# Performance work log

Measured on AMD Instinct MI355X. Metric: run time of the kernel, lower is better.

The kernel has to match this reference:

```python
import jax, jax.numpy as jnp
import numpy as np
import math

SEQ = 16384      # total ragged tokens
DIM = 1280       # vision hidden size
HEADS = 16
HDIM = DIM // HEADS  # 80
NSEG = 16        # number of segments (images); equal lengths of 1024


def rotate_half(x):
    x1, x2 = jnp.split(x, 2, axis=-1)
    return jnp.concatenate([-x2, x1], axis=-1)


def setup_inputs() -> dict:
    key = jax.random.key(0)
    ks = jax.random.split(key, 6)
    hidden_states = jax.random.normal(ks[0], (SEQ, DIM), dtype=jnp.float32)
    # rotary tables over the full head_dim (Qwen vision style: freqs duplicated)
    inv_freq = 1.0 / (10000.0 ** (jnp.arange(0, HDIM, 2, dtype=jnp.float32) / HDIM))
    pos = jnp.arange(SEQ, dtype=jnp.float32)
    freqs = jnp.outer(pos, inv_freq)                      # [S, HDIM/2]
    emb = jnp.concatenate([freqs, freqs], axis=-1)        # [S, HDIM]
    cos, sin = jnp.cos(emb), jnp.sin(emb)
    w_qkv = jax.random.normal(ks[1], (3 * DIM, DIM), dtype=jnp.float32) * 0.02
    b_qkv = jax.random.normal(ks[2], (3 * DIM,), dtype=jnp.float32) * 0.02
    w_proj = jax.random.normal(ks[3], (DIM, DIM), dtype=jnp.float32) * 0.02
    b_proj = jax.random.normal(ks[4], (DIM,), dtype=jnp.float32) * 0.02
    cu_seqlens = jnp.arange(NSEG + 1, dtype=jnp.int32) * (SEQ // NSEG)
    return {"hidden_states": hidden_states, "cos": cos, "sin": sin,
            "w_qkv": w_qkv, "b_qkv": b_qkv, "w_proj": w_proj, "b_proj": b_proj,
            "cu_seqlens": cu_seqlens}


def reference(hidden_states, cos, sin, w_qkv, b_qkv, w_proj, b_proj, cu_seqlens):
    S, D = hidden_states.shape
    hd = cos.shape[-1]
    nh = D // hd
    nseg = cu_seqlens.shape[0] - 1
    L = S // nseg  # equal segment lengths (matches cu_seqlens built in setup)

    qkv = hidden_states @ w_qkv.T + b_qkv                 # [S, 3D]
    qkv = qkv.reshape(S, 3, nh, hd)
    q, k, v = qkv[:, 0], qkv[:, 1], qkv[:, 2]             # [S, H, hd]

    # rotary (computed in float32, as in the original)
    c = cos[:, None, :]
    s = sin[:, None, :]
    q = q * c + rotate_half(q) * s
    k = k * c + rotate_half(k) * s

    # block-diagonal attention: reshape ragged-equal segments into a batch dim
    qs = q.reshape(nseg, L, nh, hd)
    ks = k.reshape(nseg, L, nh, hd)
    vs = v.reshape(nseg, L, nh, hd)

    scale = 1.0 / math.sqrt(hd)
    scores = jnp.einsum('bqhd,bkhd->bhqk', qs, ks) * scale   # [nseg, H, L, L]
    probs = jax.nn.softmax(scores, axis=-1)
    out = jnp.einsum('bhqk,bkhd->bqhd', probs, vs)           # [nseg, L, H, hd]
    out = out.reshape(S, D)
    return out @ w_proj.T + b_proj
```

## Files before the change

### kernel.cpp

```cpp
#include <hip/hip_runtime.h>

#define SEQ 16384
#define DIM 1280
#define NH 16
#define HD 80
#define NSEG 16
#define SEGL 1024

typedef __attribute__((ext_vector_type(8))) short bf16x8;
typedef __attribute__((ext_vector_type(4))) float f32x4;

__device__ inline unsigned short f2bf(float f){
  unsigned int x = __builtin_bit_cast(unsigned int, f);
  unsigned int r = (x + 0x7FFFu + ((x >> 16) & 1u)) >> 16;
  return (unsigned short)r;
}
__device__ inline float bf2f(unsigned short u){
  unsigned int x = ((unsigned int)u) << 16;
  return __builtin_bit_cast(float, x);
}
__device__ inline int cvtpk_bf16(float lo, float hi){
  int r;
  asm("v_cvt_pk_bf16_f32 %0, %1, %2" : "=v"(r) : "v"(lo), "v"(hi));
  return r;
}

__device__ inline void gload16(const unsigned short* g, unsigned short* l){
  __builtin_amdgcn_global_load_lds((const __attribute__((address_space(1))) void*)g,
                                   (__attribute__((address_space(3))) void*)l, 16, 0, 0);
}

__global__ __launch_bounds__(256) void pack_bf16_kernel(const float* __restrict__ src,
                                                        unsigned short* __restrict__ dst, int n4){
  int i = blockIdx.x * 256 + threadIdx.x;
  if (i >= n4) return;
  float4 v = ((const float4*)src)[i];
  ushort4 o;
  o.x = f2bf(v.x); o.y = f2bf(v.y); o.z = f2bf(v.z); o.w = f2bf(v.w);
  ((ushort4*)dst)[i] = o;
}

template<int EPI>
__global__ __launch_bounds__(512, 2) void gemm256_kernel(const unsigned short* __restrict__ A,
    const unsigned short* __restrict__ B, const float* __restrict__ bias,
    void* __restrict__ Cout, int M, int N, int K){
  __shared__ __attribute__((aligned(16))) unsigned short As[2][16384];
  __shared__ __attribute__((aligned(16))) unsigned short Bs[2][16384];
  const int nwg = gridDim.x;
  int bid = blockIdx.x;
  int swz = (bid & 7) * (nwg >> 3) + (bid >> 3);
  const int ntn = N >> 8;
  const int tm = (swz / ntn) << 8;
  const int tn = (swz % ntn) << 8;
  const int tid = threadIdx.x;
  const int wid = tid >> 6, l = tid & 63;
  const int lr = l & 15, lh = l >> 4;
  const int wrM = (wid >> 2) << 7;
  const int wcN = (wid & 3) << 6;
  const int NITER = K >> 7;

  const int srow = wid*8 + (l >> 3);
  const int scol = ((l & 7) ^ (l >> 3)) << 3;
  const int sldsu = wid << 9;

  const unsigned short* Ag = A + (size_t)tm * K;
  const unsigned short* Bg = B + (size_t)tn * K;

  const int ck0 = (lh*8) ^ ((l & 7) << 3);
  const int ck1 = (32 + lh*8) ^ ((l & 7) << 3);
  const int raA = (wrM + lr) << 6;
  const int raB = (wcN + lr) << 6;

  f32x4 zf = {0.f,0.f,0.f,0.f};
  f32x4 acc[8][4];
  #pragma unroll
  for (int i=0;i<8;i++)
    #pragma unroll
    for (int j=0;j<4;j++) acc[i][j] = zf;

#define STAGE_A(tile, h, q) gload16(Ag + (size_t)((h)*128 + (q)*64 + srow)*K + ((tile)<<6) + scol, \
                                    &As[(tile)&1][(h)*8192 + (q)*4096 + sldsu])
#define STAGE_B(tile, h, q) gload16(Bg + (size_t)((h)*128 + (q)*64 + srow)*K + ((tile)<<6) + scol, \
                                    &Bs[(tile)&1][(h)*8192 + (q)*4096 + sldsu])
#define RD_A(b, MOFF) \
  _Pragma("unroll") \
  for (int mi=0; mi<4; ++mi){ \
    a[0][mi] = *(const bf16x8*)&As[b][raA + ((MOFF)+mi)*1024 + ck0]; \
    a[1][mi] = *(const bf16x8*)&As[b][raA + ((MOFF)+mi)*1024 + ck1]; }
#define RD_B(b, NOFF, BREG) \
  _Pragma("unroll") \
  for (int nj=0; nj<2; ++nj){ \
    BREG[0][nj] = *(const bf16x8*)&Bs[b][raB + ((NOFF)+nj)*1024 + ck0]; \
    BREG[1][nj] = *(const bf16x8*)&Bs[b][raB + ((NOFF)+nj)*1024 + ck1]; }
#define PH_BAR() __builtin_amdgcn_s_barrier(); \
  asm volatile("s_waitcnt lgkmcnt(0)" ::: "memory"); \
  __builtin_amdgcn_sched_barrier(0);
#define QMFMA(MB, NB, BREG) \
  __builtin_amdgcn_s_setprio(1); \
  _Pragma("unroll") \
  for (int mi=0; mi<4; ++mi){ \
    _Pragma("unroll") \
    for (int nj=0; nj<2; ++nj){ \
      acc[(MB)+mi][(NB)+nj] = __builtin_amdgcn_mfma_f32_16x16x32_bf16(a[0][mi], BREG[0][nj], acc[(MB)+mi][(NB)+nj], 0,0,0); \
      acc[(MB)+mi][(NB)+nj] = __builtin_amdgcn_mfma_f32_16x16x32_bf16(a[1][mi], BREG[1][nj], acc[(MB)+mi][(NB)+nj], 0,0,0); \
    } \
  } \
  __builtin_amdgcn_s_setprio(0); \
  __builtin_amdgcn_s_barrier();

  #pragma unroll
  for (int q=0;q<2;q++){ STAGE_A(0,0,q); }
  #pragma unroll
  for (int q=0;q<2;q++){ STAGE_A(0,1,q); }
  #pragma unroll
  for (int q=0;q<2;q++){ STAGE_B(0,0,q); }
  #pragma unroll
  for (int q=0;q<2;q++){ STAGE_B(0,1,q); }
  #pragma unroll
  for (int q=0;q<2;q++){ STAGE_B(1,0,q); }
  #pragma unroll
  for (int q=0;q<2;q++){ STAGE_B(1,1,q); }
  asm volatile("s_waitcnt vmcnt(4)" ::: "memory");
  __builtin_amdgcn_s_barrier();

  for (int i=0; i<NITER; ++i){
    const int T = 2*i;
    const bool st = (i+1 < NITER);
    bf16x8 a[2][4], bx[2][2], by[2][2];

    RD_A(0, 0); RD_B(0, 0, bx);
    STAGE_A(T+1, 0, 0); STAGE_A(T+1, 0, 1);
    PH_BAR(); QMFMA(0, 0, bx);

    RD_B(0, 2, by);
    STAGE_A(T+1, 1, 0); STAGE_A(T+1, 1, 1);
    PH_BAR(); QMFMA(0, 2, by);

    RD_A(0, 4);
    if (st){ STAGE_B(T+2, 0, 0); STAGE_B(T+2, 0, 1); }
    PH_BAR(); QMFMA(4, 2, by);

    if (st){
      STAGE_B(T+2, 1, 0); STAGE_B(T+2, 1, 1);
      asm volatile("s_waitcnt vmcnt(4)" ::: "memory");
    } else {
      asm volatile("s_waitcnt vmcnt(0)" ::: "memory");
    }
    PH_BAR(); QMFMA(4, 0, bx);

    RD_A(1, 0); RD_B(1, 0, bx);
    if (st){ STAGE_A(T+2, 0, 0); STAGE_A(T+2, 0, 1); }
    PH_BAR(); QMFMA(0, 0, bx);

    RD_B(1, 2, by);
    if (st){ STAGE_A(T+2, 1, 0); STAGE_A(T+2, 1, 1); }
    PH_BAR(); QMFMA(0, 2, by);

    RD_A(1, 4);
    if (st){ STAGE_B(T+3, 0, 0); STAGE_B(T+3, 0, 1); }
    PH_BAR(); QMFMA(4, 2, by);

    if (st){
      STAGE_B(T+3, 1, 0); STAGE_B(T+3, 1, 1);
      asm volatile("s_waitcnt vmcnt(4)" ::: "memory");
    }
    PH_BAR(); QMFMA(4, 0, bx);
  }

#undef STAGE_A
#undef STAGE_B
#undef RD_A
#undef RD_B
#undef PH_BAR
#undef QMFMA

  #pragma unroll
  for (int nj=0;nj<4;nj++){
    int col = tn + wcN + nj*16 + lr;
    float bv = bias[col];
    if (EPI == 0){
      unsigned short* Q = (unsigned short*)Cout;
      int which = col / DIM;
      int rem = col - which*DIM;
      int hh = rem / HD;
      int d = rem - hh*HD;
      size_t base = (size_t)(which*NH + hh) * SEQ;
      #pragma unroll
      for (int mi=0;mi<8;mi++){
        #pragma unroll
        for (int r=0;r<4;r++){
          int row = tm + wrM + mi*16 + lh*4 + r;
          Q[(base + row)*HD + d] = f2bf(acc[mi][nj][r] + bv);
        }
      }
    } else {
      float* C = (float*)Cout;
      #pragma unroll
      for (int mi=0;mi<8;mi++){
        #pragma unroll
        for (int r=0;r<4;r++){
          int row = tm + wrM + mi*16 + lh*4 + r;
          C[(size_t)row*N + col] = acc[mi][nj][r] + bv;
        }
      }
    }
  }
}

__global__ __launch_bounds__(256) void rope_kernel(unsigned short* __restrict__ QKV,
    const float* __restrict__ cosb, const float* __restrict__ sinb){
  unsigned int gid = blockIdx.x * 256 + threadIdx.x;
  int pd = gid % 40;
  unsigned int row = gid / 40;
  int s = row % SEQ;
  float f = (row < (unsigned)(NH*SEQ)) ? (0.111803398874989485f * 1.4426950408889634f) : 1.0f;
  unsigned short* p = QKV + (size_t)row * HD;
  float c  = cosb[s*HD + pd];
  float sn = sinb[s*HD + pd];
  float x1 = bf2f(p[pd]);
  float x2 = bf2f(p[pd+40]);
  p[pd]    = f2bf((x1*c - x2*sn)*f);
  p[pd+40] = f2bf((x2*c + x1*sn)*f);
}

__global__ __launch_bounds__(256) void transpose_v_kernel(const unsigned short* __restrict__ V,
                                                          unsigned short* __restrict__ Vt){
  __shared__ unsigned short L[64*84];
  int bid = blockIdx.x;
  int h  = bid >> 8;
  int st = bid & 255;
  int s0 = st * 64;
  int tid = threadIdx.x;
  const unsigned short* Vs = V + (size_t)h * SEQ * HD;
  #pragma unroll
  for (int i=0;i<3;i++){
    int u = i*256 + tid;
    if (u < 640){
      int r = u / 10, c = u % 10;
      uint4 v = *(const uint4*)(Vs + (size_t)(s0 + r)*HD + c*8);
      unsigned int* p = (unsigned int*)&L[r*84 + c*8];
      p[0] = v.x; p[1] = v.y; p[2] = v.z; p[3] = v.w;
    }
  }
  __syncthreads();
  unsigned short* Vd = Vt + (size_t)h * HD * SEQ;
  #pragma unroll
  for (int i=0;i<5;i++){
    int u = i*256 + tid;
    int d = u >> 4, g = u & 15;
    int sb = g*4;
    int pg = ((g>>3)<<3) + ((g&3)<<1) + ((g>>2)&1);
    unsigned int w0 = (unsigned int)L[(sb+0)*84 + d] | ((unsigned int)L[(sb+1)*84 + d] << 16);
    unsigned int w1 = (unsigned int)L[(sb+2)*84 + d] | ((unsigned int)L[(sb+3)*84 + d] << 16);
    uint2 o = {w0, w1};
    *(uint2*)(Vd + (size_t)d*SEQ + s0 + pg*4) = o;
  }
}

__global__ __launch_bounds__(512) void attn_kernel(const unsigned short* __restrict__ QKV,
                                                   const unsigned short* __restrict__ Vt,
                                                   unsigned short* __restrict__ AO){
  int bid = blockIdx.x;
  int qt  = bid & 7;
  int h   = (bid >> 3) & 15;
  int seg = bid >> 7;
  int tid = threadIdx.x, wid = tid >> 6, l = tid & 63;
  int lr = l & 15, lh = l >> 4;
  const unsigned short* Qb = QKV + (size_t)(0*NH + h) * SEQ * HD;
  const unsigned short* Kb = QKV + (size_t)(1*NH + h) * SEQ * HD;
  const unsigned short* Vtb = Vt + (size_t)h * HD * SEQ;
  int q0 = seg*SEGL + qt*128;
  __shared__ __attribute__((aligned(16))) unsigned short Ksm[5152];
  __shared__ __attribute__((aligned(16))) unsigned short Vtsm[5120];
  bf16x8 qf[3];
  {
    const unsigned short* qp = Qb + (size_t)(q0 + wid*16 + lr) * HD;
    #pragma unroll
    for (int c=0;c<3;c++){
      int d0 = c*32 + lh*8;
      bf16x8 z = {0,0,0,0,0,0,0,0};
      qf[c] = (d0 < HD) ? *(const bf16x8*)(qp + d0) : z;
    }
  }
  f32x4 zf = {0.f,0.f,0.f,0.f};
  f32x4 o[5];
  #pragma unroll
  for (int dt=0;dt<5;dt++) o[dt] = zf;
  float m = -1e30f, lsum = 0.f;
  for (int kt=0; kt<16; kt++){
    int k0 = seg*SEGL + kt*64;
    const unsigned short* Ksrc = Kb + (size_t)k0 * HD;
    gload16(Ksrc + (wid*64 + l)*8, &Ksm[wid*512]);
    if (wid < 2){
      gload16(Ksrc + (512 + wid*64 + l)*8, &Ksm[4096 + wid*512]);
    } else {
      int uv = (wid-2)*64 + l;
      int d = uv >> 3, c16 = uv & 7;
      gload16(Vtb + (size_t)d*SEQ + k0 + ((c16 ^ (d & 7)) << 3), &Vtsm[(wid-2)*512]);
    }
    if (wid < 4){
      int uv = 384 + wid*64 + l;
      int d = uv >> 3, c16 = uv & 7;
      gload16(Vtb + (size_t)d*SEQ + k0 + ((c16 ^ (d & 7)) << 3), &Vtsm[3072 + wid*512]);
    }
    __syncthreads();
    f32x4 s[4];
    #pragma unroll
    for (int n=0;n<4;n++) s[n] = zf;
    #pragma unroll
    for (int c=0;c<3;c++){
      #pragma unroll
      for (int n=0;n<4;n++){
        bf16x8 kf = *(const bf16x8*)&Ksm[(n*16+lr)*80 + c*32 + lh*8];
        s[n] = __builtin_amdgcn_mfma_f32_16x16x32_bf16(kf, qf[c], s[n], 0,0,0);
      }
    }
    float pm = s[0][0];
    #pragma unroll
    for (int n=0;n<4;n++)
      #pragma unroll
      for (int r=0;r<4;r++) pm = fmaxf(pm, s[n][r]);
    pm = fmaxf(pm, __shfl_xor(pm, 16));
    pm = fmaxf(pm, __shfl_xor(pm, 32));
    if (!__all(pm <= m + 8.f)){
      float mn = fmaxf(m, pm);
      float corr = exp2f(m - mn);
      lsum *= corr;
      #pragma unroll
      for (int dt=0;dt<5;dt++)
        #pragma unroll
        for (int r=0;r<4;r++) o[dt][r] *= corr;
      m = mn;
    }
    float rs = 0.f;
    #pragma unroll
    for (int n=0;n<4;n++)
      #pragma unroll
      for (int r=0;r<4;r++){
        float p = exp2f(s[n][r] - m);
        s[n][r] = p;
        rs += p;
      }
    rs += __shfl_xor(rs, 16);
    rs += __shfl_xor(rs, 32);
    lsum += rs;
    int w[8];
    #pragma unroll
    for (int n=0;n<4;n++){
      w[2*n]   = cvtpk_bf16(s[n][0], s[n][1]);
      w[2*n+1] = cvtpk_bf16(s[n][2], s[n][3]);
    }
    #pragma unroll
    for (int kc=0;kc<2;kc++){
      union { bf16x8 v; int u[4]; } pf;
      pf.u[0] = w[4*kc+0]; pf.u[1] = w[4*kc+1];
      pf.u[2] = w[4*kc+2]; pf.u[3] = w[4*kc+3];
      #pragma unroll
      for (int dt=0;dt<5;dt++){
        int row = dt*16 + lr;
        bf16x8 vf = *(const bf16x8*)&Vtsm[row*64 + ((kc*32 + lh*8) ^ ((lr & 7) << 3))];
        o[dt] = __builtin_amdgcn_mfma_f32_16x16x32_bf16(vf, pf.v, o[dt], 0,0,0);
      }
    }
    __syncthreads();
  }
  float inv = 1.0f / lsum;
  int qrow = q0 + wid*16 + lr;
  unsigned short* op = AO + (size_t)qrow*DIM + h*HD;
  #pragma unroll
  for (int dt=0;dt<5;dt++){
    unsigned int w0 = (unsigned int)cvtpk_bf16(o[dt][0]*inv, o[dt][1]*inv);
    unsigned int w1 = (unsigned int)cvtpk_bf16(o[dt][2]*inv, o[dt][3]*inv);
    uint2 ov = {w0, w1};
    *(uint2*)(op + dt*16 + lh*4) = ov;
  }
}

extern "C" void kernel_launch(void* const* d_in, const int* in_sizes, int n_in,
                              void* d_out, int out_size, void* d_ws, size_t ws_size,
                              hipStream_t stream){
  const float* hs    = (const float*)d_in[0];
  const float* cosb  = (const float*)d_in[1];
  const float* sinb  = (const float*)d_in[2];
  const float* wqkv  = (const float*)d_in[3];
  const float* bqkv  = (const float*)d_in[4];
  const float* wproj = (const float*)d_in[5];
  const float* bproj = (const float*)d_in[6];
  float* out = (float*)d_out;

  unsigned short* Abf    = (unsigned short*)d_ws;
  unsigned short* Wqkvb  = Abf + (size_t)SEQ*DIM;
  unsigned short* Wprojb = Wqkvb + (size_t)3*DIM*DIM;
  unsigned short* QKVb   = Wprojb + (size_t)DIM*DIM;
  unsigned short* Vtb    = QKVb + (size_t)3*SEQ*DIM;
  unsigned short* AObf   = Abf;

  pack_bf16_kernel<<<(SEQ*DIM/4)/256, 256, 0, stream>>>(hs, Abf, SEQ*DIM/4);
  pack_bf16_kernel<<<(3*DIM*DIM/4)/256, 256, 0, stream>>>(wqkv, Wqkvb, 3*DIM*DIM/4);
  pack_bf16_kernel<<<(DIM*DIM/4)/256, 256, 0, stream>>>(wproj, Wprojb, DIM*DIM/4);

  gemm256_kernel<0><<<(SEQ/256)*((3*DIM)/256), 512, 0, stream>>>(Abf, Wqkvb, bqkv,
                                                                 (void*)QKVb, SEQ, 3*DIM, DIM);

  rope_kernel<<<(2*NH*SEQ*40)/256, 256, 0, stream>>>(QKVb, cosb, sinb);

  transpose_v_kernel<<<NH*(SEQ/64), 256, 0, stream>>>(QKVb + (size_t)2*NH*SEQ*HD, Vtb);

  attn_kernel<<<NSEG*NH*(SEGL/128), 512, 0, stream>>>(QKVb, Vtb, AObf);

  gemm256_kernel<1><<<(SEQ/256)*(DIM/256), 512, 0, stream>>>(AObf, Wprojb, bproj,
                                                             (void*)out, SEQ, DIM, DIM);
}
```

Measured before the change: 494.9 us.

## Deepen GEMM global-load prefetch and drop per-phase LDS waitcnt fences

Reorders the global-to-LDS staging in the 8-phase MFMA GEMM loop so A tiles for the next iteration are issued earlier, with a deeper prologue and larger vmcnt allowances. It also removes the explicit lgkmcnt(0) wait and sched_barrier after each phase barrier, letting the compiler interleave LDS reads with MFMAs. The aim is more overlap of memory latency with matrix math, at the risk of LDS read/write hazards on the double buffers if the barrier and waitcnt placement no longer covers every stage.

```diff
diff --git a/kernel.cpp b/kernel.cpp
--- a/kernel.cpp
+++ b/kernel.cpp
@@ -92,9 +92,7 @@
   for (int nj=0; nj<2; ++nj){ \
     BREG[0][nj] = *(const bf16x8*)&Bs[b][raB + ((NOFF)+nj)*1024 + ck0]; \
     BREG[1][nj] = *(const bf16x8*)&Bs[b][raB + ((NOFF)+nj)*1024 + ck1]; }
-#define PH_BAR() __builtin_amdgcn_s_barrier(); \
-  asm volatile("s_waitcnt lgkmcnt(0)" ::: "memory"); \
-  __builtin_amdgcn_sched_barrier(0);
+#define BAR() __builtin_amdgcn_s_barrier();
 #define QMFMA(MB, NB, BREG) \
   __builtin_amdgcn_s_setprio(1); \
   _Pragma("unroll") \
@@ -120,7 +118,11 @@
   for (int q=0;q<2;q++){ STAGE_B(1,0,q); }
   #pragma unroll
   for (int q=0;q<2;q++){ STAGE_B(1,1,q); }
-  asm volatile("s_waitcnt vmcnt(4)" ::: "memory");
+  #pragma unroll
+  for (int q=0;q<2;q++){ STAGE_A(1,0,q); }
+  #pragma unroll
+  for (int q=0;q<2;q++){ STAGE_A(1,1,q); }
+  asm volatile("s_waitcnt vmcnt(8)" ::: "memory");
   __builtin_amdgcn_s_barrier();
 
   for (int i=0; i<NITER; ++i){
@@ -128,50 +130,48 @@
     const bool st = (i+1 < NITER);
     bf16x8 a[2][4], bx[2][2], by[2][2];
 
-    RD_A(0, 0); RD_B(0, 0, bx);
-    STAGE_A(T+1, 0, 0); STAGE_A(T+1, 0, 1);
-    PH_BAR(); QMFMA(0, 0, bx);
+    RD_B(0, 0, bx); RD_A(0, 0);
+    BAR(); QMFMA(0, 0, bx);
 
     RD_B(0, 2, by);
-    STAGE_A(T+1, 1, 0); STAGE_A(T+1, 1, 1);
-    PH_BAR(); QMFMA(0, 2, by);
+    BAR(); QMFMA(0, 2, by);
 
     RD_A(0, 4);
     if (st){ STAGE_B(T+2, 0, 0); STAGE_B(T+2, 0, 1); }
-    PH_BAR(); QMFMA(4, 2, by);
+    BAR(); QMFMA(4, 2, by);
 
     if (st){
       STAGE_B(T+2, 1, 0); STAGE_B(T+2, 1, 1);
-      asm volatile("s_waitcnt vmcnt(4)" ::: "memory");
+      STAGE_A(T+2, 0, 0); STAGE_A(T+2, 0, 1);
+      asm volatile("s_waitcnt vmcnt(6)" ::: "memory");
     } else {
       asm volatile("s_waitcnt vmcnt(0)" ::: "memory");
     }
-    PH_BAR(); QMFMA(4, 0, bx);
-
-    RD_A(1, 0); RD_B(1, 0, bx);
-    if (st){ STAGE_A(T+2, 0, 0); STAGE_A(T+2, 0, 1); }
-    PH_BAR(); QMFMA(0, 0, bx);
+    BAR(); QMFMA(4, 0, bx);
+
+    RD_B(1, 0, bx); RD_A(1, 0);
+    if (st){ STAGE_A(T+2, 1, 0); STAGE_A(T+2, 1, 1); }
+    BAR(); QMFMA(0, 0, bx);
 
     RD_B(1, 2, by);
-    if (st){ STAGE_A(T+2, 1, 0); STAGE_A(T+2, 1, 1); }
-    PH_BAR(); QMFMA(0, 2, by);
+    BAR(); QMFMA(0, 2, by);
 
     RD_A(1, 4);
-    if (st){ STAGE_B(T+3, 0, 0); STAGE_B(T+3, 0, 1); }
-    PH_BAR(); QMFMA(4, 2, by);
+    if (st){ STAGE_B(T+3, 0, 0); STAGE_B(T+3, 0, 1); STAGE_B(T+3, 1, 0); STAGE_B(T+3, 1, 1); }
+    BAR(); QMFMA(4, 2, by);
 
     if (st){
-      STAGE_B(T+3, 1, 0); STAGE_B(T+3, 1, 1);
-      asm volatile("s_waitcnt vmcnt(4)" ::: "memory");
-    }
-    PH_BAR(); QMFMA(4, 0, bx);
+      STAGE_A(T+3, 0, 0); STAGE_A(T+3, 0, 1); STAGE_A(T+3, 1, 0); STAGE_A(T+3, 1, 1);
+      asm volatile("s_waitcnt vmcnt(8)" ::: "memory");
+    }
+    BAR(); QMFMA(4, 0, bx);
   }
 
 #undef STAGE_A
 #undef STAGE_B
 #undef RD_A
 #undef RD_B
-#undef PH_BAR
+#undef BAR
 #undef QMFMA
 
   #pragma unroll
```

Result: no change. 496.0 us (+0.2%).
